# Performance work log

Hardware: AMD Instinct MI355X
Metric: run time of the kernel (lower is better)

Reference implementation:

```python
import jax, jax.numpy as jnp
import numpy as np

B, T = 128, 512
V, E, U, K = 50000, 100, 128, 32


def _lstm(x, Wk, Wr, b):
    # x: [B, T, D] -> [B, T, U], Keras LSTM gate order i,f,g,o
    Bd = x.shape[0]
    Ud = Wr.shape[0]
    xs = jnp.swapaxes(x, 0, 1)  # [T, B, D]

    def step(carry, xt):
        h, c = carry
        z = xt @ Wk + h @ Wr + b
        i, f, g, o = jnp.split(z, 4, axis=-1)
        c = jax.nn.sigmoid(f) * c + jax.nn.sigmoid(i) * jnp.tanh(g)
        h = jax.nn.sigmoid(o) * jnp.tanh(c)
        return (h, c), h

    init = (jnp.zeros((Bd, Ud), x.dtype), jnp.zeros((Bd, Ud), x.dtype))
    _, hs = jax.lax.scan(step, init, xs)
    return jnp.swapaxes(hs, 0, 1)


def _crf_logZ(em, trans):
    # em: [B, T, K] emissions; trans: [K, K]. Forward algorithm log-partition.
    alpha0 = em[:, 0]  # [B, K]
    es = jnp.swapaxes(em[:, 1:], 0, 1)  # [T-1, B, K]

    def step(alpha, et):
        # alpha[b, i] + trans[i, j] -> logsumexp over i, plus emission
        alpha = jax.nn.logsumexp(alpha[:, :, None] + trans[None], axis=1) + et
        return alpha, None

    alphaT, _ = jax.lax.scan(step, alpha0, es)
    return jax.nn.logsumexp(alphaT, axis=-1)  # [B]


def setup_inputs() -> dict:
    key = jax.random.key(0)
    ks = jax.random.split(key, 11)
    s = 0.1
    return {
        "tokens": jax.random.randint(ks[0], (B, T), 0, V, dtype=jnp.int32),
        "emb": jax.random.normal(ks[1], (V, E), jnp.float32) * s,
        "Wk_f": jax.random.normal(ks[2], (E, 4 * U), jnp.float32) * s,
        "Wr_f": jax.random.normal(ks[3], (U, 4 * U), jnp.float32) * s,
        "b_f": jnp.zeros((4 * U,), jnp.float32),
        "Wk_b": jax.random.normal(ks[4], (E, 4 * U), jnp.float32) * s,
        "Wr_b": jax.random.normal(ks[5], (U, 4 * U), jnp.float32) * s,
        "b_b": jnp.zeros((4 * U,), jnp.float32),
        "crf_kernel": jax.random.normal(ks[6], (2 * U, K), jnp.float32) * s,
        "crf_bias": jnp.zeros((K,), jnp.float32),
        "trans": jax.random.normal(ks[7], (K, K), jnp.float32) * s,
    }


def reference(tokens, emb, Wk_f, Wr_f, b_f, Wk_b, Wr_b, b_b, crf_kernel, crf_bias, trans):
    x = emb[tokens]  # [B, T, E]
    h_f = _lstm(x, Wk_f, Wr_f, b_f)
    h_b = _lstm(x[:, ::-1], Wk_b, Wr_b, b_b)[:, ::-1]
    h = jnp.concatenate([h_f, h_b], axis=-1)  # [B, T, 2U] (dropout = identity at inference)
    em = h @ crf_kernel + crf_bias  # [B, T, K] CRF emission potentials
    return _crf_logZ(em, trans)  # [B] log-partition via CRF forward DP
```

## Files before the change

### kernel.cpp

```cpp
#include <hip/hip_runtime.h>
#include <hip/hip_bf16.h>

#define B_  128
#define T_  512
#define V_  50000
#define VP  50016
#define E_  100
#define U_  128
#define K_  32
#define G4  512
#define KP  128

typedef _Float16 h2_t __attribute__((ext_vector_type(2)));
typedef _Float16 f16x8 __attribute__((ext_vector_type(8)));
typedef __fp16   h2raw_t __attribute__((ext_vector_type(2)));
typedef short    bf16x8 __attribute__((ext_vector_type(8)));
typedef float    f32x4  __attribute__((ext_vector_type(4)));

__device__ __forceinline__ h2_t pk2(float a, float b) {
    h2raw_t r = __builtin_amdgcn_cvt_pkrtz(a, b);
    union { h2raw_t r; h2_t h; } u; u.r = r; return u.h;
}

#if __has_builtin(__builtin_amdgcn_rcpf)
__device__ __forceinline__ float rcp_f(float x) { return __builtin_amdgcn_rcpf(x); }
#else
__device__ __forceinline__ float rcp_f(float x) { return 1.f / x; }
#endif

__device__ __forceinline__ unsigned short bf16_bits(float v) {
    __hip_bfloat16 b = __float2bfloat16(v);
    union { __hip_bfloat16 b; unsigned short s; } u; u.b = b; return u.s;
}
__device__ __forceinline__ float bf2f(unsigned short u) {
    union { unsigned int i; float f; } x; x.i = ((unsigned int)u) << 16; return x.f;
}

__global__ __launch_bounds__(128) void pack_b_kernel(
    const float* __restrict__ Wk_f, const float* __restrict__ Wk_b,
    __hip_bfloat16* __restrict__ Bb)
{
    const int n = blockIdx.x;
    const int k = threadIdx.x;
    float v = 0.f;
    if (k < E_) v = (n < 512) ? Wk_f[k * 512 + n] : Wk_b[k * 512 + (n - 512)];
    Bb[n * KP + k] = __float2bfloat16(v);
}

__global__ __launch_bounds__(256, 2) void proj_mfma_kernel(
    const float* __restrict__ emb,
    const __hip_bfloat16* __restrict__ Bb,
    const float* __restrict__ b_f, const float* __restrict__ b_b,
    __hip_bfloat16* __restrict__ proj)
{
    const int r0   = blockIdx.x * 32;
    const int tid  = threadIdx.x;
    const int wv   = tid >> 6;
    const int lane = tid & 63;
    const int quad = lane >> 4;
    const int l16  = lane & 15;

    __shared__ __align__(16) float C_lds[32][268];
    unsigned short* A_st = (unsigned short*)&C_lds[0][0];

    for (int idx = tid; idx < 32 * 64; idx += 256) {
        int r = idx >> 6, kk = idx & 63;
        int vr = r0 + r; if (vr >= V_) vr = V_ - 1;
        unsigned int w = 0;
        if (kk < 50) {
            float2 v = *(const float2*)(emb + (long long)vr * E_ + 2 * kk);
            w = ((unsigned int)bf16_bits(v.y) << 16) | bf16_bits(v.x);
        }
        *(unsigned int*)&A_st[r * 136 + 2 * kk] = w;
    }
    __syncthreads();

    bf16x8 af[2][4];
    #pragma unroll
    for (int mt = 0; mt < 2; ++mt)
        #pragma unroll
        for (int kc = 0; kc < 4; ++kc)
            af[mt][kc] = *(const bf16x8*)&A_st[(mt * 16 + l16) * 136 +
                                               kc * 32 + quad * 8];
    __syncthreads();

    const unsigned short* Bu = (const unsigned short*)Bb;

    for (int ng = 0; ng < 4; ++ng) {
        const int n0 = ng * 256;

        bf16x8 bfr[4][4];
        #pragma unroll
        for (int nt = 0; nt < 4; ++nt)
            #pragma unroll
            for (int kc = 0; kc < 4; ++kc)
                bfr[nt][kc] = *(const bf16x8*)(Bu +
                    (n0 + wv * 64 + nt * 16 + l16) * KP + kc * 32 + quad * 8);

        f32x4 acc[2][4];
        #pragma unroll
        for (int mt = 0; mt < 2; ++mt)
            #pragma unroll
            for (int nt = 0; nt < 4; ++nt)
                acc[mt][nt] = (f32x4){0.f, 0.f, 0.f, 0.f};

        #pragma unroll
        for (int mt = 0; mt < 2; ++mt)
            #pragma unroll
            for (int nt = 0; nt < 4; ++nt)
                #pragma unroll
                for (int kc = 0; kc < 4; ++kc)
                    acc[mt][nt] = __builtin_amdgcn_mfma_f32_16x16x32_bf16(
                        af[mt][kc], bfr[nt][kc], acc[mt][nt], 0, 0, 0);

        #pragma unroll
        for (int mt = 0; mt < 2; ++mt)
            #pragma unroll
            for (int nt = 0; nt < 4; ++nt)
                #pragma unroll
                for (int v = 0; v < 4; ++v)
                    C_lds[mt * 16 + quad * 4 + v][wv * 64 + nt * 16 + l16] =
                        acc[mt][nt][v];
        __syncthreads();

        const float* bias = (n0 < 512) ? b_f : b_b;
        const int nbase = n0 & 511;
        for (int idx = tid; idx < 32 * 128; idx += 256) {
            int r = idx >> 7, cc = (idx & 127) * 2;
            float v0 = C_lds[r][cc]     + bias[nbase + cc];
            float v1 = C_lds[r][cc + 1] + bias[nbase + cc + 1];
            unsigned int w = ((unsigned int)bf16_bits(v1) << 16) | bf16_bits(v0);
            *(unsigned int*)(proj + (long long)(r0 + r) * 1024 + n0 + cc) = w;
        }
        __syncthreads();
    }
}

__device__ __forceinline__ float sigmoid_f(float x) {
    return rcp_f(1.f + __expf(-x));
}
__device__ __forceinline__ float tanh_f(float x) {
    return 1.f - 2.f * rcp_f(__expf(2.f * x) + 1.f);
}

__global__ __launch_bounds__(512, 1) void lstm_kernel(
    const __hip_bfloat16* __restrict__ proj,
    const int* __restrict__ tokens,
    const float* __restrict__ Wr_f, const float* __restrict__ Wr_b,
    __hip_bfloat16* __restrict__ h_buf)
{
    const int bid  = blockIdx.x;
    const int dir  = bid >> 5;
    const int b0   = (bid & 31) * 4;
    const int tid  = threadIdx.x;
    const int w    = tid >> 6;
    const int lane = tid & 63;
    const int quad = lane >> 4;
    const int l16  = lane & 15;
    const int unit = 16 * w + l16;

    const float* Wr = dir ? Wr_b : Wr_f;

    union uf16 { f16x8 v; h2_t p[4]; };
    f16x8 wb[4][4];
    #pragma unroll
    for (int gq = 0; gq < 4; ++gq) {
        const int col = gq * 128 + unit;
        #pragma unroll
        for (int kc = 0; kc < 4; ++kc) {
            const int k0 = kc * 32 + quad * 8;
            uf16 u;
            #pragma unroll
            for (int jj = 0; jj < 4; ++jj)
                u.p[jj] = pk2(Wr[(k0 + 2 * jj)     * G4 + col],
                              Wr[(k0 + 2 * jj + 1) * G4 + col]);
            wb[gq][kc] = u.v;
        }
    }

    __shared__ __align__(16) _Float16      h_lds[2][4][136];
    __shared__ __align__(16) unsigned short xkb[2][4][520];
    __shared__ unsigned short tok_lds[4][512];

    for (int idx = tid; idx < 4 * 512; idx += 512) {
        int chain = idx >> 9, tt = idx & 511;
        int tsrc = dir ? (T_ - 1 - tt) : tt;
        tok_lds[chain][tt] = (unsigned short)tokens[(b0 + chain) * T_ + tsrc];
    }
    for (int idx = tid; idx < 4 * 136; idx += 512)
        ((_Float16*)h_lds[0])[idx] = (_Float16)0.f;
    __syncthreads();

    const int sc = tid >> 7;
    const int sj = tid & 127;
    const unsigned short* prbase = (const unsigned short*)proj + dir * 512;

    int v[4][2];
    #pragma unroll
    for (int d = 0; d < 4; ++d) {
        int tk = tok_lds[sc][d];
        const unsigned int* p32 = (const unsigned int*)(prbase + (size_t)tk * 1024);
        v[d][0] = p32[sj];
        v[d][1] = p32[sj + 128];
    }
    *(unsigned int*)&xkb[0][sc][2 * sj]       = v[0][0];
    *(unsigned int*)&xkb[0][sc][2 * sj + 256] = v[0][1];
    __syncthreads();

    float c = 0.f;

    for (int t4 = 0; t4 < T_ / 4; ++t4) {
        #pragma unroll
        for (int u = 0; u < 4; ++u) {
            const int t  = t4 * 4 + u;
            const int cb = u & 1, nb = cb ^ 1;

            f16x8 a[4];
            #pragma unroll
            for (int kc = 0; kc < 4; ++kc)
                a[kc] = *(const f16x8*)&h_lds[cb][l16 >> 2][kc * 32 + quad * 8];
            unsigned short xk[4];
            #pragma unroll
            for (int gq = 0; gq < 4; ++gq)
                xk[gq] = xkb[cb][quad][gq * 128 + unit];

            {
                int tnx = t + 4; if (tnx > T_ - 1) tnx = T_ - 1;
                int tk = tok_lds[sc][tnx];
                const unsigned int* p32 =
                    (const unsigned int*)(prbase + (size_t)tk * 1024);
                v[u][0] = p32[sj];
                v[u][1] = p32[sj + 128];
            }

            f32x4 acc[4];
            #pragma unroll
            for (int gq = 0; gq < 4; ++gq)
                acc[gq] = (f32x4){0.f, 0.f, 0.f, 0.f};
            #pragma unroll
            for (int gq = 0; gq < 4; ++gq)
                #pragma unroll
                for (int kc = 0; kc < 4; ++kc)
                    acc[gq] = __builtin_amdgcn_mfma_f32_16x16x32_f16(
                        a[kc], wb[gq][kc], acc[gq], 0, 0, 0);

            float zi = acc[0][0] + bf2f(xk[0]);
            float zf = acc[1][0] + bf2f(xk[1]);
            float zg = acc[2][0] + bf2f(xk[2]);
            float zo = acc[3][0] + bf2f(xk[3]);
            c = sigmoid_f(zf) * c + sigmoid_f(zi) * tanh_f(zg);
            float h = sigmoid_f(zo) * tanh_f(c);
            h_lds[nb][quad][unit] = (_Float16)h;

            const int ttime = dir ? (T_ - 1 - t) : t;
            h_buf[((size_t)(b0 + quad) * T_ + ttime) * 256 + dir * 128 + unit] =
                __float2bfloat16(h);

            {
                const int pw = (u + 1) & 3;
                *(unsigned int*)&xkb[nb][sc][2 * sj]       = v[pw][0];
                *(unsigned int*)&xkb[nb][sc][2 * sj + 256] = v[pw][1];
            }

            asm volatile("s_waitcnt lgkmcnt(0)" ::: "memory");
            __builtin_amdgcn_s_barrier();
            asm volatile("" ::: "memory");
        }
    }
}

__global__ __launch_bounds__(256) void em_kernel(
    const __hip_bfloat16* __restrict__ h_buf,
    const float* __restrict__ ck, const float* __restrict__ cb,
    float* __restrict__ em)
{
    const int tid  = threadIdx.x;
    const int part = tid >> 5;
    const int k    = tid & 31;

    float ckr[32];
    #pragma unroll
    for (int i = 0; i < 32; ++i)
        ckr[i] = ck[(part * 32 + i) * K_ + k];
    const float cbk = cb[k];

    __shared__ float h_l[8][256];
    __shared__ float part_l[8][8][K_];

    const int r0 = blockIdx.x * 64;

    for (int round = 0; round < 8; ++round) {
        const int rbase = r0 + round * 8;
        #pragma unroll
        for (int j = 0; j < 8; ++j)
            h_l[j][tid] = __bfloat162float(h_buf[(long long)(rbase + j) * 256 + tid]);
        __syncthreads();

        #pragma unroll
        for (int j = 0; j < 8; ++j) {
            float pp = 0.f;
            #pragma unroll
            for (int i = 0; i < 32; ++i)
                pp = fmaf(h_l[j][part * 32 + i], ckr[i], pp);
            part_l[j][part][k] = pp;
        }
        __syncthreads();

        {
            int j2 = tid >> 5;
            float e = cbk;
            #pragma unroll
            for (int pq = 0; pq < 8; ++pq) e += part_l[j2][pq][k];
            em[(long long)(rbase + j2) * K_ + k] = e;
        }
        __syncthreads();
    }
}

#define PF_ 8
__global__ __launch_bounds__(64) void crf_kernel(
    const float* __restrict__ em,
    const float* __restrict__ trans,
    float* __restrict__ out)
{
    const int b    = blockIdx.x;
    const int lane = threadIdx.x;
    const int k    = lane & 31;
    const int half = lane >> 5;

    float etr[16];
    #pragma unroll
    for (int i = 0; i < 16; ++i)
        etr[i] = __expf(trans[(half * 16 + i) * K_ + k]);

    const float* em_b = em + (long long)b * T_ * K_;

    float ep[PF_];
    #pragma unroll
    for (int d = 0; d < PF_; ++d)
        ep[d] = em_b[d * K_ + k];

    float w = 0.f;
    float L = 0.f;
    for (int tb = 0; tb < T_; tb += PF_) {
        float en[PF_];
        if (tb + PF_ < T_) {
            #pragma unroll
            for (int d = 0; d < PF_; ++d)
                en[d] = em_b[(tb + PF_ + d) * K_ + k];
        } else {
            #pragma unroll
            for (int d = 0; d < PF_; ++d) en[d] = 0.f;
        }

        float eem[PF_];
        #pragma unroll
        for (int d = 0; d < PF_; ++d) eem[d] = __expf(ep[d]);

        #pragma unroll
        for (int d = 0; d < PF_; ++d) {
            if (tb + d == 0) {
                w = eem[d];
            } else {
                float acc = 0.f;
                #pragma unroll
                for (int i = 0; i < 16; ++i) {
                    float wv = __shfl(w, half * 16 + i, 64);
                    acc = fmaf(wv, etr[i], acc);
                }
                acc += __shfl_xor(acc, 32, 64);
                w = acc * eem[d];
            }
        }

        {
            float w0 = __shfl(w, 0, 64);
            w *= rcp_f(w0);
            L += __logf(w0);
        }

        #pragma unroll
        for (int d = 0; d < PF_; ++d) ep[d] = en[d];
    }

    float s = w;
    #pragma unroll
    for (int d = 1; d < 32; d <<= 1)
        s += __shfl_xor(s, d, 64);
    if (lane == 0) out[b] = L + __logf(s);
}

extern "C" void kernel_launch(void* const* d_in, const int* in_sizes, int n_in,
                              void* d_out, int out_size, void* d_ws, size_t ws_size,
                              hipStream_t stream)
{
    const int*   tokens = (const int*)  d_in[0];
    const float* emb    = (const float*)d_in[1];
    const float* Wk_f   = (const float*)d_in[2];
    const float* Wr_f   = (const float*)d_in[3];
    const float* b_f    = (const float*)d_in[4];
    const float* Wk_b   = (const float*)d_in[5];
    const float* Wr_b   = (const float*)d_in[6];
    const float* b_b    = (const float*)d_in[7];
    const float* ck     = (const float*)d_in[8];
    const float* cb     = (const float*)d_in[9];
    const float* trans  = (const float*)d_in[10];
    float* out = (float*)d_out;

    const long long ROWS = (long long)B_ * T_;
    __hip_bfloat16* proj  = (__hip_bfloat16*)d_ws;
    __hip_bfloat16* h_buf = proj + (long long)VP * 1024;
    float* em = (float*)(h_buf + ROWS * 256);
    __hip_bfloat16* Bb = (__hip_bfloat16*)(em + ROWS * K_);

    hipLaunchKernelGGL(pack_b_kernel, dim3(1024), dim3(128), 0, stream,
                       Wk_f, Wk_b, Bb);
    hipLaunchKernelGGL(proj_mfma_kernel, dim3(VP / 32), dim3(256), 0, stream,
                       emb, Bb, b_f, b_b, proj);
    hipLaunchKernelGGL(lstm_kernel, dim3(64), dim3(512), 0, stream,
                       proj, tokens, Wr_f, Wr_b, h_buf);
    hipLaunchKernelGGL(em_kernel, dim3((int)(ROWS / 64)), dim3(256), 0, stream,
                       h_buf, ck, cb, em);
    hipLaunchKernelGGL(crf_kernel, dim3(B_), dim3(64), 0, stream,
                       em, trans, out);
}
```

Before: 534.3 us.

## Fold bias into GEMM via ones column and store MFMA results directly

The bias is packed as an extra K row of the bf16 weight matrix, and a constant 1.0 is written into column 100 of the embedding tile, so the MFMA computes x·W + b in one pass. This removes the LDS staging of accumulators, the separate bias-add pass and the block-wide barriers. Blocks now cover 64 rows with 512 threads, each wave owning one 16-row tile and half the output columns. The trade-off is that writes go straight from the MFMA accumulator layout as scattered 2-byte stores, which may coalesce worse than the old packed 4-byte row writes, and the bias is rounded to bf16 before the add.

Result: slower. 590.4 us (+10.5%).

```diff
diff --git a/kernel.cpp b/kernel.cpp
--- a/kernel.cpp
+++ b/kernel.cpp
@@ -38,101 +38,75 @@
 
 __global__ __launch_bounds__(128) void pack_b_kernel(
     const float* __restrict__ Wk_f, const float* __restrict__ Wk_b,
+    const float* __restrict__ b_f, const float* __restrict__ b_b,
     __hip_bfloat16* __restrict__ Bb)
 {
     const int n = blockIdx.x;
     const int k = threadIdx.x;
     float v = 0.f;
-    if (k < E_) v = (n < 512) ? Wk_f[k * 512 + n] : Wk_b[k * 512 + (n - 512)];
+    if (k < E_)       v = (n < 512) ? Wk_f[k * 512 + n] : Wk_b[k * 512 + (n - 512)];
+    else if (k == E_) v = (n < 512) ? b_f[n]            : b_b[n - 512];
     Bb[n * KP + k] = __float2bfloat16(v);
 }
 
-__global__ __launch_bounds__(256, 2) void proj_mfma_kernel(
+__global__ __launch_bounds__(512, 1) void proj_mfma_kernel(
     const float* __restrict__ emb,
     const __hip_bfloat16* __restrict__ Bb,
-    const float* __restrict__ b_f, const float* __restrict__ b_b,
     __hip_bfloat16* __restrict__ proj)
 {
-    const int r0   = blockIdx.x * 32;
+    const int r0   = blockIdx.x * 64;
     const int tid  = threadIdx.x;
-    const int wv   = tid >> 6;
+    const int w    = tid >> 6;
     const int lane = tid & 63;
     const int quad = lane >> 4;
     const int l16  = lane & 15;
-
-    __shared__ __align__(16) float C_lds[32][268];
-    unsigned short* A_st = (unsigned short*)&C_lds[0][0];
-
-    for (int idx = tid; idx < 32 * 64; idx += 256) {
+    const int mt   = w & 3;
+    const int nh   = w >> 2;
+
+    __shared__ __align__(16) unsigned short A_st[64][136];
+
+    for (int idx = tid; idx < 64 * 64; idx += 512) {
         int r = idx >> 6, kk = idx & 63;
         int vr = r0 + r; if (vr >= V_) vr = V_ - 1;
-        unsigned int w = 0;
+        unsigned int wd = 0;
         if (kk < 50) {
             float2 v = *(const float2*)(emb + (long long)vr * E_ + 2 * kk);
-            w = ((unsigned int)bf16_bits(v.y) << 16) | bf16_bits(v.x);
-        }
-        *(unsigned int*)&A_st[r * 136 + 2 * kk] = w;
+            wd = ((unsigned int)bf16_bits(v.y) << 16) | bf16_bits(v.x);
+        } else if (kk == 50) {
+            wd = 0x3F80u;
+        }
+        *(unsigned int*)&A_st[r][2 * kk] = wd;
     }
     __syncthreads();
 
-    bf16x8 af[2][4];
-    #pragma unroll
-    for (int mt = 0; mt < 2; ++mt)
+    bf16x8 af[4];
+    #pragma unroll
+    for (int kc = 0; kc < 4; ++kc)
+        af[kc] = *(const bf16x8*)&A_st[mt * 16 + l16][kc * 32 + quad * 8];
+
+    const unsigned short* Bu = (const unsigned short*)Bb;
+
+    #pragma unroll 2
+    for (int nt = 0; nt < 32; ++nt) {
+        const int n0 = nh * 512 + nt * 16;
+
+        bf16x8 bfr[4];
         #pragma unroll
         for (int kc = 0; kc < 4; ++kc)
-            af[mt][kc] = *(const bf16x8*)&A_st[(mt * 16 + l16) * 136 +
-                                               kc * 32 + quad * 8];
-    __syncthreads();
-
-    const unsigned short* Bu = (const unsigned short*)Bb;
-
-    for (int ng = 0; ng < 4; ++ng) {
-        const int n0 = ng * 256;
-
-        bf16x8 bfr[4][4];
-        #pragma unroll
-        for (int nt = 0; nt < 4; ++nt)
-            #pragma unroll
-            for (int kc = 0; kc < 4; ++kc)
-                bfr[nt][kc] = *(const bf16x8*)(Bu +
-                    (n0 + wv * 64 + nt * 16 + l16) * KP + kc * 32 + quad * 8);
-
-        f32x4 acc[2][4];
-        #pragma unroll
-        for (int mt = 0; mt < 2; ++mt)
-            #pragma unroll
-            for (int nt = 0; nt < 4; ++nt)
-                acc[mt][nt] = (f32x4){0.f, 0.f, 0.f, 0.f};
-
-        #pragma unroll
-        for (int mt = 0; mt < 2; ++mt)
-            #pragma unroll
-            for (int nt = 0; nt < 4; ++nt)
-                #pragma unroll
-                for (int kc = 0; kc < 4; ++kc)
-                    acc[mt][nt] = __builtin_amdgcn_mfma_f32_16x16x32_bf16(
-                        af[mt][kc], bfr[nt][kc], acc[mt][nt], 0, 0, 0);
-
-        #pragma unroll
-        for (int mt = 0; mt < 2; ++mt)
-            #pragma unroll
-            for (int nt = 0; nt < 4; ++nt)
-                #pragma unroll
-                for (int v = 0; v < 4; ++v)
-                    C_lds[mt * 16 + quad * 4 + v][wv * 64 + nt * 16 + l16] =
-                        acc[mt][nt][v];
-        __syncthreads();
-
-        const float* bias = (n0 < 512) ? b_f : b_b;
-        const int nbase = n0 & 511;
-        for (int idx = tid; idx < 32 * 128; idx += 256) {
-            int r = idx >> 7, cc = (idx & 127) * 2;
-            float v0 = C_lds[r][cc]     + bias[nbase + cc];
-            float v1 = C_lds[r][cc + 1] + bias[nbase + cc + 1];
-            unsigned int w = ((unsigned int)bf16_bits(v1) << 16) | bf16_bits(v0);
-            *(unsigned int*)(proj + (long long)(r0 + r) * 1024 + n0 + cc) = w;
-        }
-        __syncthreads();
+            bfr[kc] = *(const bf16x8*)(Bu + (n0 + l16) * KP + kc * 32 + quad * 8);
+
+        f32x4 acc = (f32x4){0.f, 0.f, 0.f, 0.f};
+        #pragma unroll
+        for (int kc = 0; kc < 4; ++kc)
+            acc = __builtin_amdgcn_mfma_f32_16x16x32_bf16(
+                af[kc], bfr[kc], acc, 0, 0, 0);
+
+        #pragma unroll
+        for (int v = 0; v < 4; ++v) {
+            int row = r0 + mt * 16 + quad * 4 + v;
+            if (row > VP - 1) row = VP - 1;
+            proj[(long long)row * 1024 + n0 + l16] = __float2bfloat16(acc[v]);
+        }
     }
 }
 
@@ -414,9 +388,9 @@
     __hip_bfloat16* Bb = (__hip_bfloat16*)(em + ROWS * K_);
 
     hipLaunchKernelGGL(pack_b_kernel, dim3(1024), dim3(128), 0, stream,
-                       Wk_f, Wk_b, Bb);
-    hipLaunchKernelGGL(proj_mfma_kernel, dim3(VP / 32), dim3(256), 0, stream,
-                       emb, Bb, b_f, b_b, proj);
+                       Wk_f, Wk_b, b_f, b_b, Bb);
+    hipLaunchKernelGGL(proj_mfma_kernel, dim3((VP + 63) / 64), dim3(512), 0, stream,
+                       emb, Bb, proj);
     hipLaunchKernelGGL(lstm_kernel, dim3(64), dim3(512), 0, stream,
                        proj, tokens, Wr_f, Wr_b, h_buf);
     hipLaunchKernelGGL(em_kernel, dim3((int)(ROWS / 64)), dim3(256), 0, stream,
```
